# Kernel optimization log

Measured on AMD Instinct MI355X. Metric: run time of the kernel, lower is better.

Reference implementation:

```python
import jax, jax.numpy as jnp
import numpy as np

N_NODES = 100000
N_EDGES = 1600000
D_IN = 64
D_H1 = 64
D_H2 = 64
D_OUT = 64


def setup_inputs() -> dict:
    key = jax.random.key(0)
    ks = jax.random.split(key, 8)
    x = jax.random.normal(ks[0], (N_NODES, D_IN), dtype=jnp.float32)
    edge_index = jax.random.randint(ks[1], (2, N_EDGES), 0, N_NODES, dtype=jnp.int64)
    s1 = 1.0 / np.sqrt(D_IN)
    s2 = 1.0 / np.sqrt(D_H1)
    s3 = 1.0 / np.sqrt(D_H2)
    W1 = jax.random.uniform(ks[2], (D_IN, D_H1), jnp.float32, -s1, s1)
    b1 = jnp.zeros((D_H1,), jnp.float32)
    W2 = jax.random.uniform(ks[3], (D_H1, D_H2), jnp.float32, -s2, s2)
    b2 = jnp.zeros((D_H2,), jnp.float32)
    Wfc = jax.random.uniform(ks[4], (D_H2, D_OUT), jnp.float32, -s3, s3)
    bfc = jax.random.uniform(ks[5], (D_OUT,), jnp.float32, -s3, s3)
    return {"x": x, "edge_index": edge_index, "W1": W1, "b1": b1,
            "W2": W2, "b2": b2, "Wfc": Wfc, "bfc": bfc}


def _gcn_conv(x, W, b, src, dst, n):
    # PyG GCNConv: h = X W; out_i = sum_{j->i} (d_j d_i)^{-1/2} h_j + b
    h = x @ W                                        # [N, d_out]
    ones = jnp.ones(src.shape[0], dtype=x.dtype)
    deg = jax.ops.segment_sum(ones, dst, num_segments=n)   # in-degree (incl. self-loop)
    dinv = jnp.where(deg > 0, jax.lax.rsqrt(deg), 0.0)
    norm = dinv[src] * dinv[dst]                     # [E]
    msg = h[src] * norm[:, None]                     # [E, d_out] gather
    out = jax.ops.segment_sum(msg, dst, num_segments=n)    # scatter-add
    return out + b


def reference(x, edge_index, W1, b1, W2, b2, Wfc, bfc):
    n = x.shape[0]
    loop = jnp.arange(n, dtype=edge_index.dtype)     # self-loops (PyG default)
    src = jnp.concatenate([edge_index[0], loop])
    dst = jnp.concatenate([edge_index[1], loop])
    h = jax.nn.relu(_gcn_conv(x, W1, b1, src, dst, n))
    h = jax.nn.relu(_gcn_conv(h, W2, b2, src, dst, n))
    o = h @ Wfc + bfc                                # [N, out_dim]
    return jnp.mean(o, axis=0, keepdims=True)        # [1, out_dim]
```

## Files before the change

### kernel.cpp

```cpp
#include <hip/hip_runtime.h>
#include <hip/hip_bf16.h>


#define NSB 256

typedef __attribute__((ext_vector_type(8))) short short8v;
typedef __attribute__((ext_vector_type(4))) float float4v;
typedef __attribute__((ext_vector_type(2))) float float2v;

__device__ __forceinline__ float b2f(unsigned short u) {
    return __uint_as_float(((unsigned)u) << 16);
}
__device__ __forceinline__ unsigned short f2b(float f) {
    unsigned u = __float_as_uint(f);
    return (unsigned short)((u + 0x7fffu + ((u >> 16) & 1u)) >> 16);
}
__device__ __forceinline__ unsigned pk2(float lo, float hi) {
    return (unsigned)f2b(lo) | ((unsigned)f2b(hi) << 16);
}
__device__ __forceinline__ int origcol(int p) { return (p & 3) * 16 + (p >> 2); }

__global__ __launch_bounds__(256) void k_bcount(const int* __restrict__ dst,
                                                unsigned* __restrict__ cntBB,
                                                int E, int nbuk, int chunk) {
    __shared__ unsigned hist[1024];
    for (int i = threadIdx.x; i < nbuk; i += 256) hist[i] = 0u;
    __syncthreads();
    int lo = blockIdx.x * chunk, hi = min(E, lo + chunk);
    for (int e = lo + threadIdx.x; e < hi; e += 256)
        atomicAdd(&hist[((unsigned)dst[e]) >> 7], 1u);
    __syncthreads();
    for (int i = threadIdx.x; i < nbuk; i += 256)
        cntBB[(size_t)blockIdx.x * nbuk + i] = hist[i];
}

__global__ __launch_bounds__(NSB) void k_block_base(unsigned* __restrict__ cntBB,
                                                    unsigned* __restrict__ btot,
                                                    int nbuk) {
    __shared__ unsigned s[NSB];
    int k = blockIdx.x;
    int t = threadIdx.x;
    unsigned v = cntBB[(size_t)t * nbuk + k];
    s[t] = v;
    __syncthreads();
    for (int off = 1; off < NSB; off <<= 1) {
        unsigned a = (t >= off) ? s[t - off] : 0u;
        __syncthreads();
        s[t] += a;
        __syncthreads();
    }
    cntBB[(size_t)t * nbuk + k] = s[t] - v;
    if (t == NSB - 1) btot[k] = s[NSB - 1];
}

__global__ __launch_bounds__(1024) void k_scan_buckets(const unsigned* __restrict__ btot,
                                                       unsigned* __restrict__ bbase,
                                                       float* __restrict__ csumR,
                                                       const float* __restrict__ b1,
                                                       const float* __restrict__ b2,
                                                       float* __restrict__ b1p,
                                                       float* __restrict__ b2p,
                                                       int nbuk) {
    __shared__ unsigned s[1024];
    int k = threadIdx.x;
    for (int i = k; i < 4096; i += 1024) csumR[i] = 0.0f;
    if (k < 64) b1p[k] = b1[origcol(k)];
    else if (k < 128) b2p[k - 64] = b2[origcol(k - 64)];
    unsigned v = (k < nbuk) ? btot[k] : 0u;
    s[k] = v;
    __syncthreads();
    for (int off = 1; off < 1024; off <<= 1) {
        unsigned a = (k >= off) ? s[k - off] : 0u;
        __syncthreads();
        s[k] += a;
        __syncthreads();
    }
    if (k < nbuk) bbase[k] = s[k] - v;
    if (k == 0) bbase[nbuk] = s[1023];
}

__global__ __launch_bounds__(256) void k_bscatter(const int* __restrict__ src,
                                                  const int* __restrict__ dst,
                                                  const unsigned* __restrict__ cntBB,
                                                  const unsigned* __restrict__ bbase,
                                                  unsigned* __restrict__ epk,
                                                  int E, int nbuk, int chunk) {
    __shared__ unsigned cur[1024];
    for (int i = threadIdx.x; i < nbuk; i += 256)
        cur[i] = bbase[i] + cntBB[(size_t)blockIdx.x * nbuk + i];
    __syncthreads();
    int lo = blockIdx.x * chunk, hi = min(E, lo + chunk);
    for (int e = lo + threadIdx.x; e < hi; e += 256) {
        unsigned d = (unsigned)dst[e];
        unsigned s = (unsigned)src[e];
        unsigned pos = atomicAdd(&cur[d >> 7], 1u);
        epk[pos] = ((d & 127u) << 17) | s;
    }
}

__global__ __launch_bounds__(256) void k_sort(const unsigned* __restrict__ bbase,
                                              const unsigned* __restrict__ epk,
                                              int* __restrict__ esrc,
                                              unsigned* __restrict__ rowptr,
                                              float* __restrict__ dinv, int N, int E) {
    __shared__ unsigned cnt[128], scn[128];
    const int k = blockIdx.x;
    const int t = threadIdx.x;
    if (t < 128) cnt[t] = 0u;
    __syncthreads();
    const unsigned lo = bbase[k], hi = bbase[k + 1];
    for (unsigned e = lo + t; e < hi; e += 256)
        atomicAdd(&cnt[epk[e] >> 17], 1u);
    __syncthreads();
    unsigned c = (t < 128) ? cnt[t] : 0u;
    if (t < 128) scn[t] = c;
    __syncthreads();
    for (int off = 1; off < 128; off <<= 1) {
        unsigned a = (t < 128 && t >= off) ? scn[t - off] : 0u;
        __syncthreads();
        if (t < 128) scn[t] += a;
        __syncthreads();
    }
    int node = (k << 7) + t;
    if (t < 128) {
        unsigned start = scn[t] - c;
        cnt[t] = start;
        if (node < N) {
            rowptr[node] = lo + start;
            dinv[node] = rsqrtf(1.0f + (float)c);
        }
    }
    if (k == gridDim.x - 1 && t == 0) rowptr[N] = (unsigned)E;
    __syncthreads();
    for (unsigned e = lo + t; e < hi; e += 256) {
        unsigned w = epk[e];
        unsigned pos = atomicAdd(&cnt[w >> 17], 1u);
        esrc[lo + pos] = (int)(w & 0x1FFFFu);
    }
}

template <int AIN>
__global__ __launch_bounds__(256) void k_gemm_mfma(const void* __restrict__ in,
                                                   const float* __restrict__ W,
                                                   const float* __restrict__ rowscale,
                                                   unsigned* __restrict__ outp,
                                                   int N) {
    __shared__ float Wl[64 * 64];
    for (int i = threadIdx.x; i < 4096; i += 256) Wl[i] = W[i];
    __syncthreads();
    const int lane = threadIdx.x & 63;
    const int wv   = threadIdx.x >> 6;
    const int lr   = lane & 15;
    const int lg   = lane >> 4;

    short8v bhi[4][2], blo[4][2];
#pragma unroll
    for (int c = 0; c < 4; ++c)
#pragma unroll
        for (int s = 0; s < 2; ++s)
#pragma unroll
            for (int j = 0; j < 8; ++j) {
                int p = 32 * s + lg * 8 + j;
                int k = AIN ? origcol(p) : p;
                float wf = Wl[k * 64 + c * 16 + lr];
                unsigned short hi = f2b(wf);
                bhi[c][s][j] = (short)hi;
                blo[c][s][j] = (short)f2b(wf - b2f(hi));
            }

    const int tiles = (N + 15) >> 4;
    for (int t = blockIdx.x * 4 + wv; t < tiles; t += gridDim.x * 4) {
        const int r0 = t << 4;
        const int arow = min(r0 + lr, N - 1);
        short8v a0, a1;
        if (AIN == 0) {
            const float* ap = (const float*)in + (size_t)arow * 64 + lg * 8;
            float4 x0 = *reinterpret_cast<const float4*>(ap);
            float4 x1 = *reinterpret_cast<const float4*>(ap + 4);
            float4 x2 = *reinterpret_cast<const float4*>(ap + 32);
            float4 x3 = *reinterpret_cast<const float4*>(ap + 36);
            a0[0] = (short)f2b(x0.x); a0[1] = (short)f2b(x0.y);
            a0[2] = (short)f2b(x0.z); a0[3] = (short)f2b(x0.w);
            a0[4] = (short)f2b(x1.x); a0[5] = (short)f2b(x1.y);
            a0[6] = (short)f2b(x1.z); a0[7] = (short)f2b(x1.w);
            a1[0] = (short)f2b(x2.x); a1[1] = (short)f2b(x2.y);
            a1[2] = (short)f2b(x2.z); a1[3] = (short)f2b(x2.w);
            a1[4] = (short)f2b(x3.x); a1[5] = (short)f2b(x3.y);
            a1[6] = (short)f2b(x3.z); a1[7] = (short)f2b(x3.w);
        } else {
            const ushort* ar = (const ushort*)in + (size_t)arow * 64;
            a0 = *reinterpret_cast<const short8v*>(ar + lg * 8);
            a1 = *reinterpret_cast<const short8v*>(ar + 32 + lg * 8);
        }

        float4v acc[4];
#pragma unroll
        for (int c = 0; c < 4; ++c) acc[c] = (float4v){0.f, 0.f, 0.f, 0.f};
#pragma unroll
        for (int c = 0; c < 4; ++c) {
            acc[c] = __builtin_amdgcn_mfma_f32_16x16x32_bf16(a0, bhi[c][0], acc[c], 0, 0, 0);
            acc[c] = __builtin_amdgcn_mfma_f32_16x16x32_bf16(a1, bhi[c][1], acc[c], 0, 0, 0);
            acc[c] = __builtin_amdgcn_mfma_f32_16x16x32_bf16(a0, blo[c][0], acc[c], 0, 0, 0);
            acc[c] = __builtin_amdgcn_mfma_f32_16x16x32_bf16(a1, blo[c][1], acc[c], 0, 0, 0);
        }

        const float4 rs4 = *reinterpret_cast<const float4*>(rowscale + min(r0 + lg * 4, N - 4));
#pragma unroll
        for (int j = 0; j < 4; ++j) {
            const int row = r0 + lg * 4 + j;
            if (row < N) {
                const float rs = (&rs4.x)[j];
                int pk = __builtin_amdgcn_cvt_pk_fp8_f32(acc[0][j] * rs, acc[1][j] * rs, 0, false);
                pk = __builtin_amdgcn_cvt_pk_fp8_f32(acc[2][j] * rs, acc[3][j] * rs, pk, true);
                outp[(size_t)row * 16 + lr] = (unsigned)pk;
            }
        }
    }
}

#define ADDF8(U, A, B, C, D)                                              \
    do {                                                                  \
        float2v _lo = __builtin_amdgcn_cvt_pk_f32_fp8((int)(U), false);   \
        float2v _hi = __builtin_amdgcn_cvt_pk_f32_fp8((int)(U), true);    \
        (A) += _lo[0]; (B) += _lo[1]; (C) += _hi[0]; (D) += _hi[1];       \
    } while (0)
#define ADD16(V)                                                          \
    do {                                                                  \
        ADDF8((V).x, a[0], a[1], a[2], a[3]);                             \
        ADDF8((V).y, a[4], a[5], a[6], a[7]);                             \
        ADDF8((V).z, a[8], a[9], a[10], a[11]);                           \
        ADDF8((V).w, a[12], a[13], a[14], a[15]);                         \
    } while (0)

template <int MODE>
__global__ __launch_bounds__(256) void k_agg_csr(const unsigned char* __restrict__ hs,
                                                 const float* __restrict__ dinv,
                                                 const unsigned* __restrict__ rowptr,
                                                 const int* __restrict__ esrc,
                                                 const float* __restrict__ biasp,
                                                 ushort* __restrict__ outr,
                                                 float* __restrict__ csumR, int N) {
    const int c = threadIdx.x & 3;
    const int grp = threadIdx.x >> 2;
    const int g = blockIdx.x * 64 + grp;
    float o[16];
#pragma unroll
    for (int v = 0; v < 16; ++v) o[v] = 0.f;
    if (g < N) {
        const uint4* hw = reinterpret_cast<const uint4*>(hs);
        unsigned k = rowptr[g], end = rowptr[g + 1];
        float a[16];
        {
            uint4 v = hw[(size_t)g * 4 + c];
            float2v l0 = __builtin_amdgcn_cvt_pk_f32_fp8((int)v.x, false);
            float2v h0 = __builtin_amdgcn_cvt_pk_f32_fp8((int)v.x, true);
            float2v l1 = __builtin_amdgcn_cvt_pk_f32_fp8((int)v.y, false);
            float2v h1 = __builtin_amdgcn_cvt_pk_f32_fp8((int)v.y, true);
            float2v l2 = __builtin_amdgcn_cvt_pk_f32_fp8((int)v.z, false);
            float2v h2 = __builtin_amdgcn_cvt_pk_f32_fp8((int)v.z, true);
            float2v l3 = __builtin_amdgcn_cvt_pk_f32_fp8((int)v.w, false);
            float2v h3 = __builtin_amdgcn_cvt_pk_f32_fp8((int)v.w, true);
            a[0] = l0[0]; a[1] = l0[1]; a[2] = h0[0]; a[3] = h0[1];
            a[4] = l1[0]; a[5] = l1[1]; a[6] = h1[0]; a[7] = h1[1];
            a[8] = l2[0]; a[9] = l2[1]; a[10] = h2[0]; a[11] = h2[1];
            a[12] = l3[0]; a[13] = l3[1]; a[14] = h3[0]; a[15] = h3[1];
        }
        for (; k + 4 <= end; k += 4) {
            int s0 = esrc[k], s1 = esrc[k + 1], s2 = esrc[k + 2], s3 = esrc[k + 3];
            uint4 v0 = hw[(size_t)s0 * 4 + c];
            uint4 v1 = hw[(size_t)s1 * 4 + c];
            uint4 v2 = hw[(size_t)s2 * 4 + c];
            uint4 v3 = hw[(size_t)s3 * 4 + c];
            ADD16(v0); ADD16(v1); ADD16(v2); ADD16(v3);
        }
        for (; k < end; ++k) {
            uint4 v = hw[(size_t)esrc[k] * 4 + c];
            ADD16(v);
        }
        const float di = dinv[g];
#pragma unroll
        for (int q = 0; q < 4; ++q) {
            float4 bv = *reinterpret_cast<const float4*>(biasp + 16 * c + 4 * q);
            o[4 * q + 0] = fmaxf(fmaf(di, a[4 * q + 0], bv.x), 0.0f);
            o[4 * q + 1] = fmaxf(fmaf(di, a[4 * q + 1], bv.y), 0.0f);
            o[4 * q + 2] = fmaxf(fmaf(di, a[4 * q + 2], bv.z), 0.0f);
            o[4 * q + 3] = fmaxf(fmaf(di, a[4 * q + 3], bv.w), 0.0f);
        }
        if (MODE == 0) {
            uint4 hv0, hv1;
            hv0.x = pk2(o[0], o[1]);  hv0.y = pk2(o[2], o[3]);
            hv0.z = pk2(o[4], o[5]);  hv0.w = pk2(o[6], o[7]);
            hv1.x = pk2(o[8], o[9]);  hv1.y = pk2(o[10], o[11]);
            hv1.z = pk2(o[12], o[13]); hv1.w = pk2(o[14], o[15]);
            *reinterpret_cast<uint4*>(outr + (size_t)g * 64 + 16 * c) = hv0;
            *reinterpret_cast<uint4*>(outr + (size_t)g * 64 + 16 * c + 8) = hv1;
        }
    }
    if (MODE == 1) {
        __shared__ float red[64][65];
#pragma unroll
        for (int v = 0; v < 16; ++v) red[grp][16 * c + v] = o[v];
        __syncthreads();
        int t = threadIdx.x;
        if (t < 64) {
            float s = 0.f;
#pragma unroll
            for (int g2 = 0; g2 < 64; ++g2) s += red[g2][t];
            unsafeAtomicAdd(&csumR[(blockIdx.x & 63) * 64 + t], s);
        }
    }
}

__global__ void k_final(const float* __restrict__ csumR, const float* __restrict__ Wfc,
                        const float* __restrict__ bfc, float* __restrict__ out, float invN) {
    __shared__ float tot[64];
    int j = threadIdx.x;
    float s = 0.0f;
#pragma unroll
    for (int r = 0; r < 64; ++r) s += csumR[r * 64 + j];
    tot[j] = s;
    __syncthreads();
    float acc = 0.0f;
#pragma unroll
    for (int p = 0; p < 64; ++p)
        acc = fmaf(tot[p] * invN, Wfc[origcol(p) * 64 + j], acc);
    out[j] = acc + bfc[j];
}

extern "C" void kernel_launch(void* const* d_in, const int* in_sizes, int n_in,
                              void* d_out, int out_size, void* d_ws, size_t ws_size,
                              hipStream_t stream) {
    const float* x   = (const float*)d_in[0];
    const int*   ei  = (const int*)d_in[1];
    const float* W1  = (const float*)d_in[2];
    const float* b1  = (const float*)d_in[3];
    const float* W2  = (const float*)d_in[4];
    const float* b2  = (const float*)d_in[5];
    const float* Wfc = (const float*)d_in[6];
    const float* bfc = (const float*)d_in[7];
    float*       out = (float*)d_out;

    const int N = in_sizes[0] / 64;
    const int E = in_sizes[1] / 2;
    const int* src = ei;
    const int* dst = ei + E;

    const int nbuk  = (N + 127) >> 7;
    const int chunk = (E + NSB - 1) / NSB;

    char* ws = (char*)d_ws;
    const size_t NBH = (size_t)N * 64;
    const size_t NBR = (size_t)N * 64 * 2;
    const size_t N4  = (((size_t)(N + 1) * 4) + 255) & ~(size_t)255;
    unsigned char* hsbuf = (unsigned char*)ws;
    ushort*   h1r    = (ushort*)(ws + NBH);
    unsigned* epk    = (unsigned*)ws;
    unsigned* cntBB  = (unsigned*)(ws + NBH);
    float*    dinv   = (float*)(ws + NBH + NBR);
    unsigned* rowptr = (unsigned*)(ws + NBH + NBR + N4);
    unsigned* bbase  = (unsigned*)(ws + NBH + NBR + 2 * N4);
    unsigned* btot   = (unsigned*)(ws + NBH + NBR + 2 * N4 + 4096);
    float*    csumR  = (float*)(ws + NBH + NBR + 2 * N4 + 8192);
    float*    b1p    = (float*)(ws + NBH + NBR + 2 * N4 + 8192 + 16384);
    float*    b2p    = b1p + 64;
    int*      esrc   = (int*)(ws + NBH + NBR + 2 * N4 + 8192 + 16384 + 512);

    k_bcount<<<NSB, 256, 0, stream>>>(dst, cntBB, E, nbuk, chunk);
    k_block_base<<<nbuk, NSB, 0, stream>>>(cntBB, btot, nbuk);
    k_scan_buckets<<<1, 1024, 0, stream>>>(btot, bbase, csumR, b1, b2, b1p, b2p, nbuk);
    k_bscatter<<<NSB, 256, 0, stream>>>(src, dst, cntBB, bbase, epk, E, nbuk, chunk);
    k_sort<<<nbuk, 256, 0, stream>>>(bbase, epk, esrc, rowptr, dinv, N, E);

    k_gemm_mfma<0><<<1024, 256, 0, stream>>>(x, W1, dinv, (unsigned*)hsbuf, N);
    k_agg_csr<0><<<(N + 63) / 64, 256, 0, stream>>>(hsbuf, dinv, rowptr, esrc, b1p,
                                                    h1r, nullptr, N);

    k_gemm_mfma<1><<<1024, 256, 0, stream>>>(h1r, W2, dinv, (unsigned*)hsbuf, N);
    k_agg_csr<1><<<(N + 63) / 64, 256, 0, stream>>>(hsbuf, dinv, rowptr, esrc, b2p,
                                                    nullptr, csumR, N);

    k_final<<<1, 64, 0, stream>>>(csumR, Wfc, bfc, out, 1.0f / (float)N);
}
```

Measured before the change: 136.4 us.

## Sort nodes by degree within each bucket to balance aggregation wavefronts

Result: slower. 145.7 us (+6.8%).

```diff
diff --git a/kernel.cpp b/kernel.cpp
--- a/kernel.cpp
+++ b/kernel.cpp
@@ -102,11 +102,14 @@
                                               const unsigned* __restrict__ epk,
                                               int* __restrict__ esrc,
                                               unsigned* __restrict__ rowptr,
-                                              float* __restrict__ dinv, int N, int E) {
+                                              float* __restrict__ dinv,
+                                              int* __restrict__ perm, int N, int E) {
     __shared__ unsigned cnt[128], scn[128];
+    __shared__ unsigned dcnt[64], dcur[64];
     const int k = blockIdx.x;
     const int t = threadIdx.x;
     if (t < 128) cnt[t] = 0u;
+    if (t >= 128 && t < 192) dcnt[t - 128] = 0u;
     __syncthreads();
     const unsigned lo = bbase[k], hi = bbase[k + 1];
     for (unsigned e = lo + t; e < hi; e += 256)
@@ -121,16 +124,33 @@
         if (t < 128) scn[t] += a;
         __syncthreads();
     }
-    int node = (k << 7) + t;
+    const int node = (k << 7) + t;
+    const int nn = min(128, N - (k << 7));
     if (t < 128) {
         unsigned start = scn[t] - c;
         cnt[t] = start;
         if (node < N) {
             rowptr[node] = lo + start;
             dinv[node] = rsqrtf(1.0f + (float)c);
+            atomicAdd(&dcnt[min(c, 63u)], 1u);
         }
     }
     if (k == gridDim.x - 1 && t == 0) rowptr[N] = (unsigned)E;
+    __syncthreads();
+    if (t < 64) {
+        unsigned v = dcnt[t];
+        unsigned acc = 0;
+        for (int b = 0; b < 64; ++b) {
+            if (b == t) break;
+            acc += dcnt[b];
+        }
+        dcur[t] = acc;
+    }
+    __syncthreads();
+    if (t < 128 && node < N) {
+        unsigned rank = atomicAdd(&dcur[min(c, 63u)], 1u);
+        perm[(k << 7) + rank] = node;
+    }
     __syncthreads();
     for (unsigned e = lo + t; e < hi; e += 256) {
         unsigned w = epk[e];
@@ -237,16 +257,18 @@
                                                  const float* __restrict__ dinv,
                                                  const unsigned* __restrict__ rowptr,
                                                  const int* __restrict__ esrc,
+                                                 const int* __restrict__ perm,
                                                  const float* __restrict__ biasp,
                                                  ushort* __restrict__ outr,
                                                  float* __restrict__ csumR, int N) {
     const int c = threadIdx.x & 3;
     const int grp = threadIdx.x >> 2;
-    const int g = blockIdx.x * 64 + grp;
+    const int gi = blockIdx.x * 64 + grp;
     float o[16];
 #pragma unroll
     for (int v = 0; v < 16; ++v) o[v] = 0.f;
-    if (g < N) {
+    if (gi < N) {
+        const int g = perm[gi];
         const uint4* hw = reinterpret_cast<const uint4*>(hs);
         unsigned k = rowptr[g], end = rowptr[g + 1];
         float a[16];
@@ -352,6 +374,7 @@
     const size_t NBH = (size_t)N * 64;
     const size_t NBR = (size_t)N * 64 * 2;
     const size_t N4  = (((size_t)(N + 1) * 4) + 255) & ~(size_t)255;
+    const size_t E4  = (((size_t)E * 4) + 255) & ~(size_t)255;
     unsigned char* hsbuf = (unsigned char*)ws;
     ushort*   h1r    = (ushort*)(ws + NBH);
     unsigned* epk    = (unsigned*)ws;
@@ -364,20 +387,21 @@
     float*    b1p    = (float*)(ws + NBH + NBR + 2 * N4 + 8192 + 16384);
     float*    b2p    = b1p + 64;
     int*      esrc   = (int*)(ws + NBH + NBR + 2 * N4 + 8192 + 16384 + 512);
+    int*      perm   = (int*)(ws + NBH + NBR + 2 * N4 + 8192 + 16384 + 512 + E4);
 
     k_bcount<<<NSB, 256, 0, stream>>>(dst, cntBB, E, nbuk, chunk);
     k_block_base<<<nbuk, NSB, 0, stream>>>(cntBB, btot, nbuk);
     k_scan_buckets<<<1, 1024, 0, stream>>>(btot, bbase, csumR, b1, b2, b1p, b2p, nbuk);
     k_bscatter<<<NSB, 256, 0, stream>>>(src, dst, cntBB, bbase, epk, E, nbuk, chunk);
-    k_sort<<<nbuk, 256, 0, stream>>>(bbase, epk, esrc, rowptr, dinv, N, E);
-
-    k_gemm_mfma<0><<<1024, 256, 0, stream>>>(x, W1, dinv, (unsigned*)hsbuf, N);
-    k_agg_csr<0><<<(N + 63) / 64, 256, 0, stream>>>(hsbuf, dinv, rowptr, esrc, b1p,
-                                                    h1r, nullptr, N);
-
-    k_gemm_mfma<1><<<1024, 256, 0, stream>>>(h1r, W2, dinv, (unsigned*)hsbuf, N);
-    k_agg_csr<1><<<(N + 63) / 64, 256, 0, stream>>>(hsbuf, dinv, rowptr, esrc, b2p,
-                                                    nullptr, csumR, N);
+    k_sort<<<nbuk, 256, 0, stream>>>(bbase, epk, esrc, rowptr, dinv, perm, N, E);
+
+    k_gemm_mfma<0><<<1568, 256, 0, stream>>>(x, W1, dinv, (unsigned*)hsbuf, N);
+    k_agg_csr<0><<<(N + 63) / 64, 256, 0, stream>>>(hsbuf, dinv, rowptr, esrc, perm,
+                                                    b1p, h1r, nullptr, N);
+
+    k_gemm_mfma<1><<<1568, 256, 0, stream>>>(h1r, W2, dinv, (unsigned*)hsbuf, N);
+    k_agg_csr<1><<<(N + 63) / 64, 256, 0, stream>>>(hsbuf, dinv, rowptr, esrc, perm,
+                                                    b2p, nullptr, csumR, N);
 
     k_final<<<1, 64, 0, stream>>>(csumR, Wfc, bfc, out, 1.0f / (float)N);
 }
```
